# Kernel tuning notes

Measured on AMD Instinct MI355X. Metric: run time of the kernel, lower is better.

## Reference

```python
import jax, jax.numpy as jnp
import numpy as np

L, B, E, H = 512, 64, 512, 1024

def setup_inputs() -> dict:
    key = jax.random.key(0)
    ks = jax.random.split(key, 10)
    scale = 1.0 / np.sqrt(E + H)  # ~torch Linear init scale
    inp = {
        "x": jax.random.normal(ks[0], (L, B, E), dtype=jnp.float32),
        "c": jnp.zeros((B, H), dtype=jnp.float32),
        "h": jnp.zeros((B, H), dtype=jnp.float32),
    }
    names = ["Wf", "bf", "Wi", "bi", "Wg", "bg", "Wo", "bo"]
    for idx, name in enumerate(names):
        k = ks[idx + 1]
        if name.startswith("W"):
            inp[name] = jax.random.normal(k, (E + H, H), dtype=jnp.float32) * scale
        else:
            inp[name] = jax.random.normal(k, (H,), dtype=jnp.float32) * scale
    return inp


def reference(x, c, h, Wf, bf, Wi, bi, Wg, bg, Wo, bo):
    # Fuse the 4 gate projections into one GEMM: same math since all 4 gates
    # consume the identical concat([x_t, h_{t-1}]) input.
    W = jnp.concatenate([Wf, Wi, Wg, Wo], axis=1)  # (E+H, 4H)
    b = jnp.concatenate([bf, bi, bg, bo])          # (4H,)

    def step(carry, x_t):
        c_prev, h_prev = carry
        xh = jnp.concatenate([x_t, h_prev], axis=-1)       # (B, E+H)
        z = xh @ W + b                                     # (B, 4H)
        f_t, i_t, g_t, o_t = jnp.split(z, 4, axis=-1)
        f_t = jax.nn.sigmoid(f_t)
        i_t = jax.nn.sigmoid(i_t)
        g_t = jnp.tanh(g_t)
        o_t = jax.nn.sigmoid(o_t)
        c_t = c_prev * f_t + i_t * g_t
        h_t = o_t * jnp.tanh(c_t)
        return (c_t, h_t), (c_t, h_t)

    (_, _), (c_full, h_full) = jax.lax.scan(step, (c, h), x)
    return c_full, h_full
```

## Files before the change

### kernel.cpp

```cpp
#include <hip/hip_runtime.h>

typedef unsigned int u32;
typedef unsigned short u16;
using u32x4 = __attribute__((ext_vector_type(4))) u32;
using f16x8 = __attribute__((ext_vector_type(8))) _Float16;
using f32x4 = __attribute__((ext_vector_type(4))) float;

#define LT 512
#define BNB 64
#define ED 512
#define HD 1024
#define OUT_HALF_BYTES ((size_t)LT * BNB * HD * 4)

#define WXP_OFF  ((size_t)0)
#define WHP_OFF  ((size_t)(4u << 20))
#define BIAS_OFF ((size_t)(12u << 20))
#define HSTG_OFF ((size_t)((12u << 20) + (16u << 10)))
#define FLAG_OFF ((size_t)((12u << 20) + (16u << 10) + (256u << 10)))

__device__ __forceinline__ u16 f2h(float f) {
  _Float16 h = (_Float16)f;
  return __builtin_bit_cast(u16, h);
}
__device__ __forceinline__ float h2f(u16 s) {
  return (float)__builtin_bit_cast(_Float16, s);
}
__device__ __forceinline__ u32 pk2(float a, float b) {
  return (u32)f2h(a) | ((u32)f2h(b) << 16);
}
__device__ __forceinline__ void glds16(const void* g, void* l) {
  using GP = const __attribute__((address_space(1))) u32*;
  using SP = __attribute__((address_space(3))) u32*;
  __builtin_amdgcn_global_load_lds((GP)g, (SP)l, 16, 0, 0);
}
__device__ __forceinline__ f32x4 mfma_f16(f16x8 a, f16x8 b, f32x4 c) {
  return __builtin_amdgcn_mfma_f32_16x16x32_f16(a, b, c, 0, 0, 0);
}
__device__ __forceinline__ float sigm(float x) { return 1.0f / (1.0f + __expf(-x)); }
__device__ __forceinline__ float tanh_(float x) { return 2.0f / (1.0f + __expf(-2.0f * x)) - 1.0f; }

__device__ __forceinline__ u32x4 ldg16_cc(const void* p) {
  u32x4 r;
  asm volatile("global_load_dwordx4 %0, %1, off sc0 sc1" : "=v"(r) : "v"(p) : "memory");
  return r;
}
__device__ __forceinline__ u32 ldg_u32_cc(const void* p) {
  u32 r;
  asm volatile("global_load_dword %0, %1, off sc0 sc1\n\ts_waitcnt vmcnt(0)"
               : "=v"(r) : "v"(p) : "memory");
  return r;
}
__device__ __forceinline__ void stg_u16_cc(void* p, u32 v) {
  asm volatile("global_store_short %0, %1, off sc0 sc1" ::"v"(p), "v"(v) : "memory");
}
__device__ __forceinline__ void stg_u32_cc(void* p, u32 v) {
  asm volatile("global_store_dword %0, %1, off sc0 sc1" ::"v"(p), "v"(v) : "memory");
}
__device__ __forceinline__ u32 ldg_u16_plain(const void* p) {
  u32 r;
  asm volatile("global_load_ushort %0, %1, off" : "=v"(r) : "v"(p) : "memory");
  return r;
}
__device__ __forceinline__ void waitv0() { asm volatile("s_waitcnt vmcnt(0)" ::: "memory"); }


__global__ void pack_wx(const float* __restrict__ Wf, const float* __restrict__ Wi,
                        const float* __restrict__ Wg, const float* __restrict__ Wo,
                        u32x4* __restrict__ dst) {
  const int id = blockIdx.x * 256 + threadIdx.x;
  const int lane = id & 63;
  const int row = id >> 6;
  const int ntile = row >> 7;
  const int rem = row & 127;
  const int kt = rem >> 3;
  const int fn = rem & 7;
  const int np = (ntile << 7) + (fn << 4) + (lane & 15);
  const int g = (np >> 4) & 3;
  const int jfull = ((np >> 6) << 4) + (np & 15);
  const int k0 = (kt << 5) + ((lane >> 4) << 3);
  const float* W = (g == 0) ? Wf : (g == 1) ? Wi : (g == 2) ? Wg : Wo;
  const float* s = W + (size_t)k0 * HD + jfull;
  u16 h[8];
#pragma unroll
  for (int i = 0; i < 8; ++i) h[i] = f2h(s[(size_t)i * HD]);
  u32x4 v;
  v[0] = (u32)h[0] | ((u32)h[1] << 16);
  v[1] = (u32)h[2] | ((u32)h[3] << 16);
  v[2] = (u32)h[4] | ((u32)h[5] << 16);
  v[3] = (u32)h[6] | ((u32)h[7] << 16);
  dst[id] = v;
}

__global__ void pack_wh(const float* __restrict__ Wf, const float* __restrict__ Wi,
                        const float* __restrict__ Wg, const float* __restrict__ Wo,
                        u32x4* __restrict__ dst) {
  const int id = blockIdx.x * 256 + threadIdx.x;
  const int lane = id & 63;
  const int row = id >> 6;
  const int cg = row >> 7;
  const int rem = row & 127;
  const int w = rem >> 5;
  const int g = (rem >> 3) & 3;
  const int kk = rem & 7;
  const int k = ED + (w << 8) + (kk << 5) + ((lane >> 4) << 3);
  const int j = (cg << 4) + (lane & 15);
  const float* W = (g == 0) ? Wf : (g == 1) ? Wi : (g == 2) ? Wg : Wo;
  const float* s = W + (size_t)k * HD + j;
  u16 h[8];
#pragma unroll
  for (int i = 0; i < 8; ++i) h[i] = f2h(s[(size_t)i * HD]);
  u32x4 v;
  v[0] = (u32)h[0] | ((u32)h[1] << 16);
  v[1] = (u32)h[2] | ((u32)h[3] << 16);
  v[2] = (u32)h[4] | ((u32)h[5] << 16);
  v[3] = (u32)h[6] | ((u32)h[7] << 16);
  dst[id] = v;
}

__global__ void pack_bias_flags(const float* __restrict__ bf, const float* __restrict__ bi,
                                const float* __restrict__ bg, const float* __restrict__ bo,
                                float* __restrict__ dst, int* __restrict__ flags) {
  const int id = blockIdx.x * 256 + threadIdx.x;
  const int g = (id >> 4) & 3;
  const int jfull = ((id >> 6) << 4) + (id & 15);
  const float* B = (g == 0) ? bf : (g == 1) ? bi : (g == 2) ? bg : bo;
  dst[id] = B[jfull];
  flags[id] = 0;
}


__global__ __launch_bounds__(256) void zx_gemm(const float* __restrict__ x,
                                               const u32x4* __restrict__ wxp,
                                               const float* __restrict__ biasp,
                                               char* __restrict__ outb) {
  __shared__ u32x4 Ab[512];
  __shared__ u32x4 Bb[512];
  const int bid = blockIdx.x;
  const int ntile = bid & 31;
  const int mtile = bid >> 5;
  const int tid = threadIdx.x;
  const int lane = tid & 63;
  const int wid = tid >> 6;
  const int wm = wid & 1;
  const int wn = wid >> 1;
  const int m0 = mtile << 7;

  const f32x4 fz = {0.f, 0.f, 0.f, 0.f};
  f32x4 acc[4][4];
#pragma unroll
  for (int i = 0; i < 4; ++i)
#pragma unroll
    for (int j = 0; j < 4; ++j) acc[i][j] = fz;

  for (int kt = 0; kt < 16; ++kt) {
#pragma unroll
    for (int r = 0; r < 2; ++r) {
      const int c = tid + (r << 8);
      const int fl = c & 63;
      const int fmg = c >> 6;
      const int row = m0 + (fmg << 4) + (fl & 15);
      const int kc = (kt << 5) + ((fl >> 4) << 3);
      const float* s = x + (size_t)row * ED + kc;
      const float4 p0 = *(const float4*)s;
      const float4 p1 = *(const float4*)(s + 4);
      u32x4 v;
      v[0] = pk2(p0.x, p0.y);
      v[1] = pk2(p0.z, p0.w);
      v[2] = pk2(p1.x, p1.y);
      v[3] = pk2(p1.z, p1.w);
      Ab[c] = v;
    }
    {
      const u32x4* bsrc = wxp + (((size_t)(ntile << 4) + kt) << 9);
#pragma unroll
      for (int r = 0; r < 2; ++r) {
        const int cb = (wid << 6) + (r << 8);
        glds16((const void*)(bsrc + cb + lane), (void*)&Bb[cb]);
      }
    }
    __syncthreads();
    f16x8 afr[4], bfr[4];
#pragma unroll
    for (int f = 0; f < 4; ++f) afr[f] = __builtin_bit_cast(f16x8, Ab[((wm * 4 + f) << 6) + lane]);
#pragma unroll
    for (int f = 0; f < 4; ++f) bfr[f] = __builtin_bit_cast(f16x8, Bb[((wn * 4 + f) << 6) + lane]);
#pragma unroll
    for (int fm = 0; fm < 4; ++fm)
#pragma unroll
      for (int fn = 0; fn < 4; ++fn) acc[fm][fn] = mfma_f16(afr[fm], bfr[fn], acc[fm][fn]);
    __syncthreads();
  }

  char* const cb_ = outb;
  char* const hb_ = outb + OUT_HALF_BYTES;
  const int r0 = (lane >> 4) << 2;
#pragma unroll
  for (int fn = 0; fn < 4; ++fn) {
    const int np = (ntile << 7) + (wn << 6) + (fn << 4) + (lane & 15);
    const float bv = biasp[np];
    const int gg = (np >> 4) & 3;
    const int cg = np >> 6;
    const int jj = np & 15;
    char* const outHalf = (gg < 2) ? cb_ : hb_;
    const size_t coloff = (size_t)(cg << 6) + ((gg & 1) << 5) + (jj << 1);
#pragma unroll
    for (int fm = 0; fm < 4; ++fm) {
#pragma unroll
      for (int r = 0; r < 4; ++r) {
        const int m = m0 + (wm << 6) + (fm << 4) + r0 + r;
        *(u16*)(outHalf + (size_t)m * 4096 + coloff) = f2h(acc[fm][fn][r] + bv);
      }
    }
  }
}


__global__ __launch_bounds__(256, 1) void lstm_rec(const float* __restrict__ c0,
                                                   const float* __restrict__ h0,
                                                   const u32x4* __restrict__ whp, char* outb,
                                                   u16* hstage, int* flags) {
  __shared__ u32x4 Ab[2048];
  __shared__ float zb[4][4][16][17];
  const int bid = blockIdx.x;
  const int mslab = bid & 3;
  const int cgp = bid >> 2;
  const int tid = threadIdx.x;
  const int lane = tid & 63;
  const int wid = tid >> 6;
  const int b_loc = tid >> 4;
  const int j_loc = tid & 15;
  const int b = (mslab << 4) + b_loc;
  const int jf = (cgp << 4) + j_loc;

  f16x8 wreg[4][8];
  {
    const u32x4* wb = whp + (((size_t)(cgp * 4 + wid)) << 11);
#pragma unroll
    for (int g = 0; g < 4; ++g)
#pragma unroll
      for (int kk = 0; kk < 8; ++kk)
        wreg[g][kk] = __builtin_bit_cast(f16x8, wb[((g << 3) + kk) * 64 + lane]);
  }
  float creg = c0[(b << 10) + jf];
  stg_u16_cc(hstage + (b << 10) + jf, (u32)f2h(h0[(b << 10) + jf]));

  char* const cb_ = outb;
  char* const hb_ = outb + OUT_HALF_BYTES;
  int* const myflag = flags + (((cgp << 2) + mslab) << 4);
  int* const pollflag = flags + ((((tid & 63) << 2) + mslab) << 4);

  waitv0();
  __syncthreads();
  if (tid == 0) stg_u32_cc(myflag, 1u);
  u32 xf16, xi16, xg16, xo16;
  {
    const size_t rowoff = ((size_t)b) << 12;
    const char* crow = cb_ + rowoff + (cgp << 6);
    const char* hrow = hb_ + rowoff + (cgp << 6);
    xf16 = ldg_u16_plain(crow + (j_loc << 1));
    xi16 = ldg_u16_plain(crow + 32 + (j_loc << 1));
    xg16 = ldg_u16_plain(hrow + (j_loc << 1));
    xo16 = ldg_u16_plain(hrow + 32 + (j_loc << 1));
  }
  if (tid < 64) {
    while ((int)ldg_u32_cc(pollflag) < 1) {}
  }
  __syncthreads();

  const f32x4 fz = {0.f, 0.f, 0.f, 0.f};
#pragma unroll 1
  for (int t = 0; t < LT; ++t) {
    const u16* hsrc = hstage + ((size_t)(t & 1) << 16);
    u32x4 hreg[8];
#pragma unroll
    for (int it = 0; it < 8; ++it) {
      const int kk = (it << 2) + wid;
      const u16* src =
          hsrc + (((mslab << 4) + (lane & 15)) << 10) + (kk << 5) + ((lane >> 4) << 3);
      hreg[it] = ldg16_cc(src);
    }
    waitv0();
    const float zx_f = h2f((u16)xf16), zx_i = h2f((u16)xi16);
    const float zx_g = h2f((u16)xg16), zx_o = h2f((u16)xo16);
#pragma unroll
    for (int it = 0; it < 8; ++it) {
      const int kk = (it << 2) + wid;
      Ab[(kk << 6) + lane] = hreg[it];
    }
    __syncthreads();

    f32x4 a0 = fz, a1 = fz, a2 = fz, a3 = fz;
#pragma unroll
    for (int kk = 0; kk < 8; ++kk) {
      const f16x8 av = __builtin_bit_cast(f16x8, Ab[((wid << 3) + kk) * 64 + lane]);
      a0 = mfma_f16(av, wreg[0][kk], a0);
      a1 = mfma_f16(av, wreg[1][kk], a1);
      a2 = mfma_f16(av, wreg[2][kk], a2);
      a3 = mfma_f16(av, wreg[3][kk], a3);
    }
    {
      const int rr = (lane >> 4) << 2;
      const int cc = lane & 15;
#pragma unroll
      for (int r = 0; r < 4; ++r) {
        zb[wid][0][rr + r][cc] = a0[r];
        zb[wid][1][rr + r][cc] = a1[r];
        zb[wid][2][rr + r][cc] = a2[r];
        zb[wid][3][rr + r][cc] = a3[r];
      }
    }
    __syncthreads();

    float zf = zx_f, zi = zx_i, zg = zx_g, zo = zx_o;
#pragma unroll
    for (int w = 0; w < 4; ++w) {
      zf += zb[w][0][b_loc][j_loc];
      zi += zb[w][1][b_loc][j_loc];
      zg += zb[w][2][b_loc][j_loc];
      zo += zb[w][3][b_loc][j_loc];
    }
    const float fgate = sigm(zf);
    const float igate = sigm(zi);
    const float ggate = tanh_(zg);
    const float ogate = sigm(zo);
    creg = creg * fgate + igate * ggate;
    const float hv = ogate * tanh_(creg);

    stg_u16_cc(hstage + ((((size_t)(t + 1)) & 1) << 16) + (b << 10) + jf, (u32)f2h(hv));
    waitv0();
    __syncthreads();
    if (tid == 0) stg_u32_cc(myflag, (u32)(t + 2));

    const size_t rowoff = ((size_t)(t * 64 + b)) << 12;
    *(float*)(cb_ + rowoff + ((size_t)jf << 2)) = creg;
    *(float*)(hb_ + rowoff + ((size_t)jf << 2)) = hv;

    {
      const int tn = (t + 1 < LT) ? t + 1 : t;
      const size_t rown = ((size_t)(tn * 64 + b)) << 12;
      const char* crow = cb_ + rown + (cgp << 6);
      const char* hrow = hb_ + rown + (cgp << 6);
      xf16 = ldg_u16_plain(crow + (j_loc << 1));
      xi16 = ldg_u16_plain(crow + 32 + (j_loc << 1));
      xg16 = ldg_u16_plain(hrow + (j_loc << 1));
      xo16 = ldg_u16_plain(hrow + 32 + (j_loc << 1));
    }
    if (tid < 64) {
      while ((int)ldg_u32_cc(pollflag) < t + 2) {}
    }
    __syncthreads();
  }
}

extern "C" void kernel_launch(void* const* d_in, const int* in_sizes, int n_in, void* d_out,
                              int out_size, void* d_ws, size_t ws_size, hipStream_t stream) {
  const float* x = (const float*)d_in[0];
  const float* c0 = (const float*)d_in[1];
  const float* h0 = (const float*)d_in[2];
  const float* Wf = (const float*)d_in[3];
  const float* bf = (const float*)d_in[4];
  const float* Wi = (const float*)d_in[5];
  const float* bi = (const float*)d_in[6];
  const float* Wg = (const float*)d_in[7];
  const float* bg = (const float*)d_in[8];
  const float* Wo = (const float*)d_in[9];
  const float* bo = (const float*)d_in[10];

  char* ws = (char*)d_ws;
  u32x4* wxp = (u32x4*)(ws + WXP_OFF);
  u32x4* whp = (u32x4*)(ws + WHP_OFF);
  float* bp = (float*)(ws + BIAS_OFF);
  u16* hstage = (u16*)(ws + HSTG_OFF);
  int* flags = (int*)(ws + FLAG_OFF);

  pack_wx<<<1024, 256, 0, stream>>>(Wf, Wi, Wg, Wo, wxp);
  pack_wh<<<2048, 256, 0, stream>>>(Wf, Wi, Wg, Wo, whp);
  pack_bias_flags<<<16, 256, 0, stream>>>(bf, bi, bg, bo, bp, flags);
  zx_gemm<<<8192, 256, 0, stream>>>(x, wxp, bp, (char*)d_out);
  lstm_rec<<<256, 256, 0, stream>>>(c0, h0, whp, (char*)d_out, hstage, flags);
}
```

Baseline: 2.290 ms.

## Replace flag-based inter-block barrier with timestep-tagged hidden-state words

Each hidden value is now stored as a 32-bit word carrying the timestep in its upper half, and consumer waves spin-read their A-fragments directly until every tag matches. This removes the per-block flag stores, the flag polling, the extra syncthreads, and the LDS staging of h. The cost is twice the global read and write traffic for the hidden state, plus a repacking step in registers. There is also a subtle correctness risk: the first step's tags rely on the initial store writing a tag of zero, and stale workspace from a previous run could falsely match.

```diff
diff --git a/kernel.cpp b/kernel.cpp
--- a/kernel.cpp
+++ b/kernel.cpp
@@ -16,7 +16,6 @@
 #define WHP_OFF  ((size_t)(4u << 20))
 #define BIAS_OFF ((size_t)(12u << 20))
 #define HSTG_OFF ((size_t)((12u << 20) + (16u << 10)))
-#define FLAG_OFF ((size_t)((12u << 20) + (16u << 10) + (256u << 10)))
 
 __device__ __forceinline__ u16 f2h(float f) {
   _Float16 h = (_Float16)f;
@@ -44,15 +43,6 @@
   asm volatile("global_load_dwordx4 %0, %1, off sc0 sc1" : "=v"(r) : "v"(p) : "memory");
   return r;
 }
-__device__ __forceinline__ u32 ldg_u32_cc(const void* p) {
-  u32 r;
-  asm volatile("global_load_dword %0, %1, off sc0 sc1\n\ts_waitcnt vmcnt(0)"
-               : "=v"(r) : "v"(p) : "memory");
-  return r;
-}
-__device__ __forceinline__ void stg_u16_cc(void* p, u32 v) {
-  asm volatile("global_store_short %0, %1, off sc0 sc1" ::"v"(p), "v"(v) : "memory");
-}
 __device__ __forceinline__ void stg_u32_cc(void* p, u32 v) {
   asm volatile("global_store_dword %0, %1, off sc0 sc1" ::"v"(p), "v"(v) : "memory");
 }
@@ -62,6 +52,15 @@
   return r;
 }
 __device__ __forceinline__ void waitv0() { asm volatile("s_waitcnt vmcnt(0)" ::: "memory"); }
+
+__device__ __forceinline__ f16x8 unpk(u32x4 lo, u32x4 hi) {
+  u32x4 w;
+  w[0] = (lo[0] & 0xFFFFu) | (lo[1] << 16);
+  w[1] = (lo[2] & 0xFFFFu) | (lo[3] << 16);
+  w[2] = (hi[0] & 0xFFFFu) | (hi[1] << 16);
+  w[3] = (hi[2] & 0xFFFFu) | (hi[3] << 16);
+  return __builtin_bit_cast(f16x8, w);
+}
 
 
 __global__ void pack_wx(const float* __restrict__ Wf, const float* __restrict__ Wi,
@@ -117,15 +116,14 @@
   dst[id] = v;
 }
 
-__global__ void pack_bias_flags(const float* __restrict__ bf, const float* __restrict__ bi,
-                                const float* __restrict__ bg, const float* __restrict__ bo,
-                                float* __restrict__ dst, int* __restrict__ flags) {
+__global__ void pack_bias(const float* __restrict__ bf, const float* __restrict__ bi,
+                          const float* __restrict__ bg, const float* __restrict__ bo,
+                          float* __restrict__ dst) {
   const int id = blockIdx.x * 256 + threadIdx.x;
   const int g = (id >> 4) & 3;
   const int jfull = ((id >> 6) << 4) + (id & 15);
   const float* B = (g == 0) ? bf : (g == 1) ? bi : (g == 2) ? bg : bo;
   dst[id] = B[jfull];
-  flags[id] = 0;
 }
 
 
@@ -218,8 +216,7 @@
 __global__ __launch_bounds__(256, 1) void lstm_rec(const float* __restrict__ c0,
                                                    const float* __restrict__ h0,
                                                    const u32x4* __restrict__ whp, char* outb,
-                                                   u16* hstage, int* flags) {
-  __shared__ u32x4 Ab[2048];
+                                                   u32* hstg) {
   __shared__ float zb[4][4][16][17];
   const int bid = blockIdx.x;
   const int mslab = bid & 3;
@@ -242,57 +239,49 @@
         wreg[g][kk] = __builtin_bit_cast(f16x8, wb[((g << 3) + kk) * 64 + lane]);
   }
   float creg = c0[(b << 10) + jf];
-  stg_u16_cc(hstage + (b << 10) + jf, (u32)f2h(h0[(b << 10) + jf]));
+  stg_u32_cc(hstg + (b << 10) + jf, (u32)f2h(h0[(b << 10) + jf]));
 
   char* const cb_ = outb;
   char* const hb_ = outb + OUT_HALF_BYTES;
-  int* const myflag = flags + (((cgp << 2) + mslab) << 4);
-  int* const pollflag = flags + ((((tid & 63) << 2) + mslab) << 4);
-
-  waitv0();
-  __syncthreads();
-  if (tid == 0) stg_u32_cc(myflag, 1u);
+
   u32 xf16, xi16, xg16, xo16;
   {
-    const size_t rowoff = ((size_t)b) << 12;
-    const char* crow = cb_ + rowoff + (cgp << 6);
-    const char* hrow = hb_ + rowoff + (cgp << 6);
+    const size_t rowb = ((size_t)b) << 12;
+    const char* crow = cb_ + rowb + (cgp << 6);
+    const char* hrow = hb_ + rowb + (cgp << 6);
     xf16 = ldg_u16_plain(crow + (j_loc << 1));
     xi16 = ldg_u16_plain(crow + 32 + (j_loc << 1));
     xg16 = ldg_u16_plain(hrow + (j_loc << 1));
     xo16 = ldg_u16_plain(hrow + 32 + (j_loc << 1));
   }
-  if (tid < 64) {
-    while ((int)ldg_u32_cc(pollflag) < 1) {}
-  }
-  __syncthreads();
+
+  const u32 aoff = (u32)((((mslab << 4) + (lane & 15)) << 10) + (wid << 8) + ((lane >> 4) << 3));
 
   const f32x4 fz = {0.f, 0.f, 0.f, 0.f};
 #pragma unroll 1
   for (int t = 0; t < LT; ++t) {
-    const u16* hsrc = hstage + ((size_t)(t & 1) << 16);
-    u32x4 hreg[8];
-#pragma unroll
-    for (int it = 0; it < 8; ++it) {
-      const int kk = (it << 2) + wid;
-      const u16* src =
-          hsrc + (((mslab << 4) + (lane & 15)) << 10) + (kk << 5) + ((lane >> 4) << 3);
-      hreg[it] = ldg16_cc(src);
-    }
-    waitv0();
-    const float zx_f = h2f((u16)xf16), zx_i = h2f((u16)xi16);
-    const float zx_g = h2f((u16)xg16), zx_o = h2f((u16)xo16);
-#pragma unroll
-    for (int it = 0; it < 8; ++it) {
-      const int kk = (it << 2) + wid;
-      Ab[(kk << 6) + lane] = hreg[it];
-    }
-    __syncthreads();
+    const u32* ab = hstg + (((u32)t & 1) << 16) + aoff;
+    const u32 gtag = (u32)t << 16;
+    u32x4 v[16];
+    for (;;) {
+#pragma unroll
+      for (int kk = 0; kk < 8; ++kk) {
+        v[2 * kk] = ldg16_cc(ab + (kk << 5));
+        v[2 * kk + 1] = ldg16_cc(ab + (kk << 5) + 4);
+      }
+      waitv0();
+      u32 acm = 0;
+#pragma unroll
+      for (int i = 0; i < 16; ++i)
+        acm |= (v[i][0] ^ gtag) | (v[i][1] ^ gtag) | (v[i][2] ^ gtag) | (v[i][3] ^ gtag);
+      if (__all(acm < 0x10000u)) break;
+      __builtin_amdgcn_s_sleep(1);
+    }
 
     f32x4 a0 = fz, a1 = fz, a2 = fz, a3 = fz;
 #pragma unroll
     for (int kk = 0; kk < 8; ++kk) {
-      const f16x8 av = __builtin_bit_cast(f16x8, Ab[((wid << 3) + kk) * 64 + lane]);
+      const f16x8 av = unpk(v[2 * kk], v[2 * kk + 1]);
       a0 = mfma_f16(av, wreg[0][kk], a0);
       a1 = mfma_f16(av, wreg[1][kk], a1);
       a2 = mfma_f16(av, wreg[2][kk], a2);
@@ -311,7 +300,8 @@
     }
     __syncthreads();
 
-    float zf = zx_f, zi = zx_i, zg = zx_g, zo = zx_o;
+    float zf = h2f((u16)xf16), zi = h2f((u16)xi16);
+    float zg = h2f((u16)xg16), zo = h2f((u16)xo16);
 #pragma unroll
     for (int w = 0; w < 4; ++w) {
       zf += zb[w][0][b_loc][j_loc];
@@ -319,25 +309,22 @@
       zg += zb[w][2][b_loc][j_loc];
       zo += zb[w][3][b_loc][j_loc];
     }
-    const float fgate = sigm(zf);
-    const float igate = sigm(zi);
-    const float ggate = tanh_(zg);
-    const float ogate = sigm(zo);
-    creg = creg * fgate + igate * ggate;
-    const float hv = ogate * tanh_(creg);
-
-    stg_u16_cc(hstage + ((((size_t)(t + 1)) & 1) << 16) + (b << 10) + jf, (u32)f2h(hv));
-    waitv0();
     __syncthreads();
-    if (tid == 0) stg_u32_cc(myflag, (u32)(t + 2));
-
-    const size_t rowoff = ((size_t)(t * 64 + b)) << 12;
+
+    const float fg = sigm(zf), ig = sigm(zi), gg = tanh_(zg), og = sigm(zo);
+    creg = creg * fg + ig * gg;
+    const float hv = og * tanh_(creg);
+
+    stg_u32_cc(hstg + ((((u32)(t + 1)) & 1) << 16) + (b << 10) + jf,
+               (((u32)(t + 1)) << 16) | (u32)f2h(hv));
+
+    const size_t rowoff = ((size_t)((t << 6) + b)) << 12;
     *(float*)(cb_ + rowoff + ((size_t)jf << 2)) = creg;
     *(float*)(hb_ + rowoff + ((size_t)jf << 2)) = hv;
 
     {
       const int tn = (t + 1 < LT) ? t + 1 : t;
-      const size_t rown = ((size_t)(tn * 64 + b)) << 12;
+      const size_t rown = ((size_t)((tn << 6) + b)) << 12;
       const char* crow = cb_ + rown + (cgp << 6);
       const char* hrow = hb_ + rown + (cgp << 6);
       xf16 = ldg_u16_plain(crow + (j_loc << 1));
@@ -345,10 +332,6 @@
       xg16 = ldg_u16_plain(hrow + (j_loc << 1));
       xo16 = ldg_u16_plain(hrow + 32 + (j_loc << 1));
     }
-    if (tid < 64) {
-      while ((int)ldg_u32_cc(pollflag) < t + 2) {}
-    }
-    __syncthreads();
   }
 }
 
@@ -370,12 +353,11 @@
   u32x4* wxp = (u32x4*)(ws + WXP_OFF);
   u32x4* whp = (u32x4*)(ws + WHP_OFF);
   float* bp = (float*)(ws + BIAS_OFF);
-  u16* hstage = (u16*)(ws + HSTG_OFF);
-  int* flags = (int*)(ws + FLAG_OFF);
+  u32* hstg = (u32*)(ws + HSTG_OFF);
 
   pack_wx<<<1024, 256, 0, stream>>>(Wf, Wi, Wg, Wo, wxp);
   pack_wh<<<2048, 256, 0, stream>>>(Wf, Wi, Wg, Wo, whp);
-  pack_bias_flags<<<16, 256, 0, stream>>>(bf, bi, bg, bo, bp, flags);
+  pack_bias<<<16, 256, 0, stream>>>(bf, bi, bg, bo, bp);
   zx_gemm<<<8192, 256, 0, stream>>>(x, wxp, bp, (char*)d_out);
-  lstm_rec<<<256, 256, 0, stream>>>(c0, h0, whp, (char*)d_out, hstage, flags);
-}
+  lstm_rec<<<256, 256, 0, stream>>>(c0, h0, whp, (char*)d_out, hstg);
+}
```

Measured after the change: 2.843 ms. +24.2%, slower.
